# Kernel tuning notes

Measured on AMD Instinct MI355X. Metric: run time of the kernel, lower is better.

The kernel has to match this reference:

```python
import jax, jax.numpy as jnp
from jax import lax
import numpy as np

B, T, C = 32, 1024, 512
K = 3
MAX_DUR = 4            # durations drawn from [0,5) -> max value 4
L_MAX = T * MAX_DUR    # static padded mel length (torch pads to batch max; we pad to static max)
EPS = 1e-5


def conv_ln_block(x, w, b, g, beta):
    # x: [B,T,C]; torch ConvLNBlock: permute -> Conv1d(SAME) -> relu -> permute -> LayerNorm -> dropout(eval=id)
    y = lax.conv_general_dilated(x.transpose(0, 2, 1), w, (1,), 'SAME',
                                 dimension_numbers=('NCH', 'OIH', 'NCH')) + b[None, :, None]
    y = jax.nn.relu(y).transpose(0, 2, 1)  # [B,T,Cout]
    mu = y.mean(-1, keepdims=True)
    var = y.var(-1, keepdims=True)
    return (y - mu) * lax.rsqrt(var + EPS) * g + beta


def regulate(batch, durations, token_lengths):
    # Vectorized equivalent of DurationRegulator.inflate: repeat token t durations[b,t] times,
    # concatenate, pad. Implemented as cumsum + searchsorted gather (single pass, no ragged loops).
    pos = jnp.arange(T)
    valid = pos[None, :] < token_lengths[:, None]          # [B,T]
    d = jnp.where(valid, durations, 0)
    total = d.sum(axis=1)
    # torch: if durs.sum()==0 -> fill with 1
    d = jnp.where((total == 0)[:, None], valid.astype(d.dtype), d)
    total = d.sum(axis=1)                                   # [B]
    cum = jnp.cumsum(d, axis=1)                             # inclusive cumsum [B,T]
    frames = jnp.arange(L_MAX)
    idx = jax.vmap(lambda c: jnp.searchsorted(c, frames, side='right'))(cum)  # [B,L_MAX]
    idx = jnp.clip(idx, 0, T - 1)
    out = jnp.take_along_axis(batch, idx[:, :, None], axis=1)                 # [B,L_MAX,C]
    frame_mask = frames[None, :] < total[:, None]
    out = out * frame_mask[:, :, None].astype(batch.dtype)
    return out, total.astype(jnp.float32)


def setup_inputs() -> dict:
    key = jax.random.key(0)
    ks = jax.random.split(key, 8)
    batch = jax.random.normal(ks[0], (B, T, C), dtype=jnp.float32)
    token_lengths = jax.random.randint(ks[1], (B,), T // 2, T + 1).astype(jnp.int32)
    mask = jnp.arange(T)[None, :] < token_lengths[:, None]
    label_durations = jax.random.randint(ks[2], (B, T), 0, MAX_DUR + 1).astype(jnp.int32)
    s1 = 1.0 / np.sqrt(C * K)
    s2 = 1.0 / np.sqrt(C * K)
    params = {
        'conv1_w': jax.random.uniform(ks[3], (C, C, K), minval=-s1, maxval=s1, dtype=jnp.float32),
        'conv1_b': jnp.zeros((C,), jnp.float32),
        'ln1_g': jnp.ones((C,), jnp.float32), 'ln1_b': jnp.zeros((C,), jnp.float32),
        'conv2_w': jax.random.uniform(ks[4], (C, C, K), minval=-s2, maxval=s2, dtype=jnp.float32),
        'conv2_b': jnp.zeros((C,), jnp.float32),
        'ln2_g': jnp.ones((C,), jnp.float32), 'ln2_b': jnp.zeros((C,), jnp.float32),
        'lin_w': jax.random.uniform(ks[5], (C, 1), minval=-1/np.sqrt(C), maxval=1/np.sqrt(C), dtype=jnp.float32),
        'lin_b': jnp.zeros((1,), jnp.float32),
    }
    return dict(batch=batch, token_lengths=token_lengths, mask=mask,
                label_durations=label_durations, **params)


def reference(batch, token_lengths, mask, label_durations,
              conv1_w, conv1_b, ln1_g, ln1_b,
              conv2_w, conv2_b, ln2_g, ln2_b,
              lin_w, lin_b):
    # VariancePredictor: two ConvLN blocks + Linear(out_channels, 1), masked fill 0
    h = conv_ln_block(batch, conv1_w, conv1_b, ln1_g, ln1_b)
    h = conv_ln_block(h, conv2_w, conv2_b, ln2_g, ln2_b)
    predicted_durations = h @ lin_w + lin_b                      # [B,T,1]
    predicted_durations = jnp.where(mask[:, :, None], predicted_durations, 0.0)
    # label_durations provided -> regulator uses labels (training path), alpha=1
    padded_batch, mel_lengths = regulate(batch, label_durations, token_lengths)
    return padded_batch, mel_lengths, predicted_durations
```

## Files before the change

### kernel.cpp

```cpp
#include <hip/hip_runtime.h>
#include <hip/hip_bf16.h>
#include <stdint.h>

typedef _Float16 f16;
typedef _Float16 f16x8 __attribute__((ext_vector_type(8)));
typedef float f32x4 __attribute__((ext_vector_type(4)));

#define B_    32
#define T_    1024
#define TP_   1026
#define C_    512
#define LMAX_ 4096
#define KDIM  1536

#define XPAD_OFF   0u
#define H1PAD_OFF  33619968u
#define W1T_OFF    67239936u
#define W2T_OFF    68812800u
#define YWS_OFF    70385664u
#define CUM_OFF    137494528u
#define TOT_OFF    137625600u
#define IDX_OFF    137625728u

#define AS1C(p) ((const __attribute__((address_space(1))) void*)(p))
#define AS3(p)  ((__attribute__((address_space(3))) void*)(p))

__global__ __launch_bounds__(256) void prep_pad(const float* __restrict__ batch,
                                                f16* __restrict__ xpad,
                                                f16* __restrict__ h1pad) {
    int row = blockIdx.x * 4 + (threadIdx.x >> 6);
    int lane = threadIdx.x & 63;
    int b = row / TP_, tt = row % TP_;
    size_t dsto = (size_t)row * C_ + lane * 8;
    if (tt == 0 || tt == TP_ - 1) {
        f16x8 z = {};
        *(f16x8*)(xpad + dsto) = z;
        *(f16x8*)(h1pad + dsto) = z;
    } else {
        const float* src = batch + ((size_t)(b * T_ + tt - 1)) * C_ + lane * 8;
        float4 v0 = ((const float4*)src)[0];
        float4 v1 = ((const float4*)src)[1];
        f16x8 h;
        h[0] = (f16)v0.x; h[1] = (f16)v0.y; h[2] = (f16)v0.z; h[3] = (f16)v0.w;
        h[4] = (f16)v1.x; h[5] = (f16)v1.y; h[6] = (f16)v1.z; h[7] = (f16)v1.w;
        *(f16x8*)(xpad + dsto) = h;
    }
}

__global__ __launch_bounds__(256) void prep_w(const float* __restrict__ w1,
                                              const float* __restrict__ w2,
                                              f16* __restrict__ w1t,
                                              f16* __restrict__ w2t) {
    int o = blockIdx.x;
    const float* w = blockIdx.y ? w2 : w1;
    f16* wt = blockIdx.y ? w2t : w1t;
    for (int j = threadIdx.x; j < KDIM; j += 256) {
        int tap = j >> 9, i = j & 511;
        wt[(size_t)o * KDIM + j] = (f16)w[(size_t)o * KDIM + i * 3 + tap];
    }
}

__global__ __launch_bounds__(1024) void scan_kernel(const int* __restrict__ dur,
                                                    const int* __restrict__ tlen,
                                                    int* __restrict__ idxarr,
                                                    int* __restrict__ total,
                                                    float* __restrict__ mel_out) {
    int b = blockIdx.x, t = threadIdx.x;
    __shared__ int sd[1024];
    __shared__ int sv[1024];
    int L = tlen[b];
    int valid = (t < L) ? 1 : 0;
    int d = valid ? dur[b * T_ + t] : 0;
    sd[t] = d; sv[t] = valid;
    __syncthreads();
    for (int off = 1; off < 1024; off <<= 1) {
        int x = 0, y = 0;
        if (t >= off) { x = sd[t - off]; y = sv[t - off]; }
        __syncthreads();
        sd[t] += x; sv[t] += y;
        __syncthreads();
    }
    int totd = sd[1023];
    int cur  = (totd == 0) ? sv[t] : sd[t];
    int prev = (t == 0) ? 0 : ((totd == 0) ? sv[t - 1] : sd[t - 1]);
    for (int f = prev; f < cur; f++) idxarr[b * LMAX_ + f] = t;
    if (t == 1023) {
        int tt = (totd == 0) ? sv[1023] : totd;
        total[b] = tt;
        mel_out[b] = (float)tt;
    }
}

__global__ __launch_bounds__(256, 2) void gemm_convln(const f16* __restrict__ A,
                                                      const f16* __restrict__ Bw,
                                                      const float* __restrict__ bias,
                                                      float* __restrict__ Y) {
    __shared__ f16 As[128 * 64];
    __shared__ f16 Bs[128 * 64];
    const int tid = threadIdx.x;
    const int lane = tid & 63;
    const int wid = tid >> 6;
    const int m0 = blockIdx.x * 128;
    const int n0 = blockIdx.y * 128;
    const int arow0 = (m0 >> 10) * TP_ + (m0 & 1023);
    const int wm = (wid & 1) * 64;
    const int wn = (wid >> 1) * 64;

    f32x4 acc[4][4];
#pragma unroll
    for (int i = 0; i < 4; i++)
#pragma unroll
        for (int j = 0; j < 4; j++) acc[i][j] = (f32x4){0.f, 0.f, 0.f, 0.f};

    const int srow = wid * 8 + (lane >> 3);
    const int gmem = (lane & 7) ^ (lane >> 3);
    const f16* aBase = A + (size_t)(arow0 + srow) * C_ + gmem * 8;
    const f16* bBase = Bw + (size_t)(n0 + srow) * KDIM + gmem * 8;

    for (int kk = 0; kk < KDIM; kk += 64) {
        __syncthreads();
#pragma unroll
        for (int i = 0; i < 4; i++) {
            __builtin_amdgcn_global_load_lds(AS1C(aBase + (size_t)(i * 32) * C_ + kk),
                                             AS3(&As[(wid * 8 + i * 32) * 64]), 16, 0, 0);
            __builtin_amdgcn_global_load_lds(AS1C(bBase + (size_t)(i * 32) * KDIM + kk),
                                             AS3(&Bs[(wid * 8 + i * 32) * 64]), 16, 0, 0);
        }
        __syncthreads();
#pragma unroll
        for (int ks = 0; ks < 2; ks++) {
            const int slot = ((ks << 2) + (lane >> 4)) ^ (lane & 7);
            f16x8 af[4], bf[4];
#pragma unroll
            for (int mi = 0; mi < 4; mi++)
                af[mi] = *(const f16x8*)&As[(wm + mi * 16 + (lane & 15)) * 64 + slot * 8];
#pragma unroll
            for (int ni = 0; ni < 4; ni++)
                bf[ni] = *(const f16x8*)&Bs[(wn + ni * 16 + (lane & 15)) * 64 + slot * 8];
#pragma unroll
            for (int mi = 0; mi < 4; mi++)
#pragma unroll
                for (int ni = 0; ni < 4; ni++)
                    acc[mi][ni] = __builtin_amdgcn_mfma_f32_16x16x32_f16(
                        af[mi], bf[ni], acc[mi][ni], 0, 0, 0);
        }
    }

    const int col = lane & 15;
    const int row4 = (lane >> 4) * 4;
#pragma unroll
    for (int ni = 0; ni < 4; ni++) {
        int n = n0 + wn + ni * 16 + col;
        float bn = bias[n];
#pragma unroll
        for (int mi = 0; mi < 4; mi++) {
#pragma unroll
            for (int r = 0; r < 4; r++) {
                int m = m0 + wm + mi * 16 + row4 + r;
                float v = acc[mi][ni][r] + bn;
                Y[(size_t)m * C_ + n] = v > 0.f ? v : 0.f;
            }
        }
    }
}

__global__ __launch_bounds__(256) void ln_kernel(const float* __restrict__ Y,
                                                 const float* __restrict__ g,
                                                 const float* __restrict__ be,
                                                 f16* __restrict__ hpad) {
    int row = blockIdx.x * 4 + (threadIdx.x >> 6);
    int lane = threadIdx.x & 63;
    const float4* y = (const float4*)(Y + (size_t)row * C_);
    float4 v0 = y[lane * 2], v1 = y[lane * 2 + 1];
    float s = v0.x + v0.y + v0.z + v0.w + v1.x + v1.y + v1.z + v1.w;
    float q = v0.x * v0.x + v0.y * v0.y + v0.z * v0.z + v0.w * v0.w +
              v1.x * v1.x + v1.y * v1.y + v1.z * v1.z + v1.w * v1.w;
#pragma unroll
    for (int m = 32; m; m >>= 1) { s += __shfl_xor(s, m, 64); q += __shfl_xor(q, m, 64); }
    float mu = s * (1.f / 512.f);
    float x = q * (1.f / 512.f) - mu * mu + 1e-5f;
    float rs = rsqrtf(x);
    rs = rs * (1.5f - 0.5f * x * rs * rs);
    const float4* g4 = (const float4*)g;
    const float4* b4 = (const float4*)be;
    float4 g0 = g4[lane * 2], g1 = g4[lane * 2 + 1];
    float4 e0 = b4[lane * 2], e1 = b4[lane * 2 + 1];
    f16x8 h;
    h[0] = (f16)((v0.x - mu) * rs * g0.x + e0.x);
    h[1] = (f16)((v0.y - mu) * rs * g0.y + e0.y);
    h[2] = (f16)((v0.z - mu) * rs * g0.z + e0.z);
    h[3] = (f16)((v0.w - mu) * rs * g0.w + e0.w);
    h[4] = (f16)((v1.x - mu) * rs * g1.x + e1.x);
    h[5] = (f16)((v1.y - mu) * rs * g1.y + e1.y);
    h[6] = (f16)((v1.z - mu) * rs * g1.z + e1.z);
    h[7] = (f16)((v1.w - mu) * rs * g1.w + e1.w);
    int b = row >> 10, t = row & 1023;
    *(f16x8*)(hpad + ((size_t)(b * TP_ + t + 1)) * C_ + lane * 8) = h;
}

__global__ __launch_bounds__(256) void ln2pred_kernel(const float* __restrict__ Y,
                                                      const float* __restrict__ g,
                                                      const float* __restrict__ be,
                                                      const float* __restrict__ lw,
                                                      const float* __restrict__ lb,
                                                      const int* __restrict__ tlen,
                                                      float* __restrict__ pred) {
    int row = blockIdx.x * 4 + (threadIdx.x >> 6);
    int lane = threadIdx.x & 63;
    const float4* y = (const float4*)(Y + (size_t)row * C_);
    float4 v0 = y[lane * 2], v1 = y[lane * 2 + 1];
    float s = v0.x + v0.y + v0.z + v0.w + v1.x + v1.y + v1.z + v1.w;
    float q = v0.x * v0.x + v0.y * v0.y + v0.z * v0.z + v0.w * v0.w +
              v1.x * v1.x + v1.y * v1.y + v1.z * v1.z + v1.w * v1.w;
#pragma unroll
    for (int m = 32; m; m >>= 1) { s += __shfl_xor(s, m, 64); q += __shfl_xor(q, m, 64); }
    float mu = s * (1.f / 512.f);
    float x = q * (1.f / 512.f) - mu * mu + 1e-5f;
    float rs = rsqrtf(x);
    rs = rs * (1.5f - 0.5f * x * rs * rs);
    const float4* g4 = (const float4*)g;
    const float4* b4 = (const float4*)be;
    const float4* w4 = (const float4*)lw;
    float4 g0 = g4[lane * 2], g1 = g4[lane * 2 + 1];
    float4 e0 = b4[lane * 2], e1 = b4[lane * 2 + 1];
    float4 w0 = w4[lane * 2], w1 = w4[lane * 2 + 1];
    float p = ((v0.x - mu) * rs * g0.x + e0.x) * w0.x +
              ((v0.y - mu) * rs * g0.y + e0.y) * w0.y +
              ((v0.z - mu) * rs * g0.z + e0.z) * w0.z +
              ((v0.w - mu) * rs * g0.w + e0.w) * w0.w +
              ((v1.x - mu) * rs * g1.x + e1.x) * w1.x +
              ((v1.y - mu) * rs * g1.y + e1.y) * w1.y +
              ((v1.z - mu) * rs * g1.z + e1.z) * w1.z +
              ((v1.w - mu) * rs * g1.w + e1.w) * w1.w;
#pragma unroll
    for (int m = 32; m; m >>= 1) p += __shfl_xor(p, m, 64);
    if (lane == 0) {
        int b = row >> 10, t = row & 1023;
        pred[row] = (t < tlen[b]) ? (p + lb[0]) : 0.f;
    }
}

__global__ __launch_bounds__(256) void gather_kernel(const float* __restrict__ batch,
                                                     const int* __restrict__ idxarr,
                                                     const int* __restrict__ total,
                                                     float* __restrict__ out) {
    int gw = blockIdx.x * 4 + (threadIdx.x >> 6);
    int lane = threadIdx.x & 63;
    int b = gw >> 12;
    int l = gw & (LMAX_ - 1);
    int tot = total[b];
    float4* dst = (float4*)(out + ((size_t)b * LMAX_ + l) * C_);
    if (l < tot) {
        int idx = idxarr[gw];
        const float4* src = (const float4*)(batch + ((size_t)b * T_ + idx) * C_);
        dst[lane] = src[lane];
        dst[lane + 64] = src[lane + 64];
    } else {
        float4 z = {0.f, 0.f, 0.f, 0.f};
        dst[lane] = z;
        dst[lane + 64] = z;
    }
}

extern "C" void kernel_launch(void* const* d_in, const int* in_sizes, int n_in,
                              void* d_out, int out_size, void* d_ws, size_t ws_size,
                              hipStream_t stream) {
    const float* batch = (const float*)d_in[0];
    const int* tlen    = (const int*)d_in[1];
    const int* durs    = (const int*)d_in[3];
    const float* w1  = (const float*)d_in[4];
    const float* b1  = (const float*)d_in[5];
    const float* g1  = (const float*)d_in[6];
    const float* be1 = (const float*)d_in[7];
    const float* w2  = (const float*)d_in[8];
    const float* b2  = (const float*)d_in[9];
    const float* g2  = (const float*)d_in[10];
    const float* be2 = (const float*)d_in[11];
    const float* lw  = (const float*)d_in[12];
    const float* lb  = (const float*)d_in[13];

    float* out      = (float*)d_out;
    float* mel_out  = out + (size_t)B_ * LMAX_ * C_;
    float* pred_out = mel_out + B_;

    char* ws    = (char*)d_ws;
    f16* xpad   = (f16*)(ws + XPAD_OFF);
    f16* h1pad  = (f16*)(ws + H1PAD_OFF);
    f16* w1t    = (f16*)(ws + W1T_OFF);
    f16* w2t    = (f16*)(ws + W2T_OFF);
    float* yws  = (float*)(ws + YWS_OFF);
    int* tot    = (int*)(ws + TOT_OFF);
    int* idxarr = (int*)(ws + IDX_OFF);

    prep_pad<<<B_ * TP_ / 4, 256, 0, stream>>>(batch, xpad, h1pad);
    prep_w<<<dim3(512, 2), 256, 0, stream>>>(w1, w2, w1t, w2t);
    scan_kernel<<<B_, 1024, 0, stream>>>(durs, tlen, idxarr, tot, mel_out);
    gemm_convln<<<dim3(256, 4), 256, 0, stream>>>(xpad, w1t, b1, yws);
    ln_kernel<<<8192, 256, 0, stream>>>(yws, g1, be1, h1pad);
    gemm_convln<<<dim3(256, 4), 256, 0, stream>>>(h1pad, w2t, b2, yws);
    ln2pred_kernel<<<8192, 256, 0, stream>>>(yws, g2, be2, lw, lb, tlen, pred_out);
    gather_kernel<<<B_ * LMAX_ / 4, 256, 0, stream>>>(batch, idxarr, tot, out);
}
```

Baseline: 489.1 us.

## Fuse LayerNorm and prediction epilogues into full-row conv GEMM tiles

Each GEMM block now computes a 64-row by full 512-column tile using 32x32x16 MFMAs, so the LayerNorm (and, in the second pass, the linear prediction head) runs in the epilogue out of a shared-memory staging buffer. The fp32 intermediate workspace and the two separate LayerNorm kernels go away, which removes a large global write and read of the activations plus two launches. In exchange, each block uses about 72KB of LDS and a larger accumulator set, and the B tile per k-step is much larger. This may reduce occupancy, and the grid shrinks to 512 blocks.

```diff
diff --git a/kernel.cpp b/kernel.cpp
--- a/kernel.cpp
+++ b/kernel.cpp
@@ -3,8 +3,10 @@
 #include <stdint.h>
 
 typedef _Float16 f16;
+typedef _Float16 f16x4v __attribute__((ext_vector_type(4)));
 typedef _Float16 f16x8 __attribute__((ext_vector_type(8)));
 typedef float f32x4 __attribute__((ext_vector_type(4)));
+typedef float f32x16 __attribute__((ext_vector_type(16)));
 
 #define B_    32
 #define T_    1024
@@ -17,10 +19,8 @@
 #define H1PAD_OFF  33619968u
 #define W1T_OFF    67239936u
 #define W2T_OFF    68812800u
-#define YWS_OFF    70385664u
-#define CUM_OFF    137494528u
-#define TOT_OFF    137625600u
-#define IDX_OFF    137625728u
+#define TOT_OFF    70385664u
+#define IDX_OFF    70385920u
 
 #define AS1C(p) ((const __attribute__((address_space(1))) void*)(p))
 #define AS3(p)  ((__attribute__((address_space(3))) void*)(p))
@@ -91,152 +91,134 @@
     }
 }
 
-__global__ __launch_bounds__(256, 2) void gemm_convln(const f16* __restrict__ A,
-                                                      const f16* __restrict__ Bw,
-                                                      const float* __restrict__ bias,
-                                                      float* __restrict__ Y) {
-    __shared__ f16 As[128 * 64];
-    __shared__ f16 Bs[128 * 64];
+template <int MODE>
+__global__ __launch_bounds__(256, 2) void fgemm(const f16* __restrict__ A,
+                                                const f16* __restrict__ Bw,
+                                                const float* __restrict__ bias,
+                                                const float* __restrict__ g,
+                                                const float* __restrict__ be,
+                                                const float* __restrict__ lw,
+                                                const float* __restrict__ lb,
+                                                const int* __restrict__ tlen,
+                                                f16* __restrict__ hpad,
+                                                float* __restrict__ pred) {
+    __shared__ __align__(16) char smem[73728];
+    f16* As = (f16*)smem;
+    f16* Bs = (f16*)(smem + 8192);
+    float* Ew = (float*)smem;
+
     const int tid = threadIdx.x;
     const int lane = tid & 63;
-    const int wid = tid >> 6;
-    const int m0 = blockIdx.x * 128;
-    const int n0 = blockIdx.y * 128;
+    const int w = tid >> 6;
+    const int m0 = blockIdx.x * 64;
     const int arow0 = (m0 >> 10) * TP_ + (m0 & 1023);
-    const int wm = (wid & 1) * 64;
-    const int wn = (wid >> 1) * 64;
-
-    f32x4 acc[4][4];
-#pragma unroll
-    for (int i = 0; i < 4; i++)
-#pragma unroll
-        for (int j = 0; j < 4; j++) acc[i][j] = (f32x4){0.f, 0.f, 0.f, 0.f};
-
-    const int srow = wid * 8 + (lane >> 3);
-    const int gmem = (lane & 7) ^ (lane >> 3);
-    const f16* aBase = A + (size_t)(arow0 + srow) * C_ + gmem * 8;
-    const f16* bBase = Bw + (size_t)(n0 + srow) * KDIM + gmem * 8;
+
+    f32x16 acc[2][4];
+#pragma unroll
+    for (int i = 0; i < 2; i++)
+#pragma unroll
+        for (int j = 0; j < 4; j++) acc[i][j] = (f32x16){};
+
+    const int srow = lane >> 3;
+    const int gran = (lane & 7) ^ srow;
+    const f16* aB = A + (size_t)(arow0 + w * 16 + srow) * C_ + gran * 8;
+    const f16* bB = Bw + (size_t)(w * 128 + srow) * KDIM + gran * 8;
 
     for (int kk = 0; kk < KDIM; kk += 64) {
         __syncthreads();
 #pragma unroll
-        for (int i = 0; i < 4; i++) {
-            __builtin_amdgcn_global_load_lds(AS1C(aBase + (size_t)(i * 32) * C_ + kk),
-                                             AS3(&As[(wid * 8 + i * 32) * 64]), 16, 0, 0);
-            __builtin_amdgcn_global_load_lds(AS1C(bBase + (size_t)(i * 32) * KDIM + kk),
-                                             AS3(&Bs[(wid * 8 + i * 32) * 64]), 16, 0, 0);
+        for (int i = 0; i < 2; i++)
+            __builtin_amdgcn_global_load_lds(AS1C(aB + (size_t)(i * 8) * C_ + kk),
+                                             AS3(&As[(w * 16 + i * 8) * 64]), 16, 0, 0);
+#pragma unroll
+        for (int j = 0; j < 16; j++)
+            __builtin_amdgcn_global_load_lds(AS1C(bB + (size_t)(j * 8) * KDIM + kk),
+                                             AS3(&Bs[(w * 128 + j * 8) * 64]), 16, 0, 0);
+        __syncthreads();
+#pragma unroll
+        for (int ks = 0; ks < 4; ks++) {
+            const int slot = (ks * 2 + (lane >> 5)) ^ (lane & 7);
+            f16x8 af[2], bf[4];
+#pragma unroll
+            for (int mt = 0; mt < 2; mt++)
+                af[mt] = *(const f16x8*)&As[(mt * 32 + (lane & 31)) * 64 + slot * 8];
+#pragma unroll
+            for (int nt = 0; nt < 4; nt++)
+                bf[nt] = *(const f16x8*)&Bs[(w * 128 + nt * 32 + (lane & 31)) * 64 + slot * 8];
+#pragma unroll
+            for (int mt = 0; mt < 2; mt++)
+#pragma unroll
+                for (int nt = 0; nt < 4; nt++)
+                    acc[mt][nt] = __builtin_amdgcn_mfma_f32_32x32x16_f16(
+                        af[mt], bf[nt], acc[mt][nt], 0, 0, 0);
         }
-        __syncthreads();
-#pragma unroll
-        for (int ks = 0; ks < 2; ks++) {
-            const int slot = ((ks << 2) + (lane >> 4)) ^ (lane & 7);
-            f16x8 af[4], bf[4];
-#pragma unroll
-            for (int mi = 0; mi < 4; mi++)
-                af[mi] = *(const f16x8*)&As[(wm + mi * 16 + (lane & 15)) * 64 + slot * 8];
-#pragma unroll
-            for (int ni = 0; ni < 4; ni++)
-                bf[ni] = *(const f16x8*)&Bs[(wn + ni * 16 + (lane & 15)) * 64 + slot * 8];
-#pragma unroll
-            for (int mi = 0; mi < 4; mi++)
-#pragma unroll
-                for (int ni = 0; ni < 4; ni++)
-                    acc[mi][ni] = __builtin_amdgcn_mfma_f32_16x16x32_f16(
-                        af[mi], bf[ni], acc[mi][ni], 0, 0, 0);
-        }
-    }
-
-    const int col = lane & 15;
-    const int row4 = (lane >> 4) * 4;
-#pragma unroll
-    for (int ni = 0; ni < 4; ni++) {
-        int n = n0 + wn + ni * 16 + col;
-        float bn = bias[n];
-#pragma unroll
-        for (int mi = 0; mi < 4; mi++) {
-#pragma unroll
-            for (int r = 0; r < 4; r++) {
-                int m = m0 + wm + mi * 16 + row4 + r;
-                float v = acc[mi][ni][r] + bn;
-                Y[(size_t)m * C_ + n] = v > 0.f ? v : 0.f;
+    }
+
+    float bcol[4];
+#pragma unroll
+    for (int nt = 0; nt < 4; nt++) bcol[nt] = bias[w * 128 + nt * 32 + (lane & 31)];
+    const float4 gA = ((const float4*)g)[lane], gB = ((const float4*)g)[64 + lane];
+    const float4 eA = ((const float4*)be)[lane], eB = ((const float4*)be)[64 + lane];
+    float4 wA, wB;
+    if (MODE == 2) { wA = ((const float4*)lw)[lane]; wB = ((const float4*)lw)[64 + lane]; }
+
+#pragma unroll
+    for (int c = 0; c < 2; c++) {
+        __syncthreads();
+#pragma unroll
+        for (int nt = 0; nt < 4; nt++) {
+            const int col = w * 128 + nt * 32 + (lane & 31);
+#pragma unroll
+            for (int reg = 0; reg < 16; reg++) {
+                const int row = (reg & 3) + 8 * (reg >> 2) + 4 * (lane >> 5);
+                float v = acc[c][nt][reg] + bcol[nt];
+                Ew[row * 512 + col] = v > 0.f ? v : 0.f;
             }
         }
-    }
-}
-
-__global__ __launch_bounds__(256) void ln_kernel(const float* __restrict__ Y,
-                                                 const float* __restrict__ g,
-                                                 const float* __restrict__ be,
-                                                 f16* __restrict__ hpad) {
-    int row = blockIdx.x * 4 + (threadIdx.x >> 6);
-    int lane = threadIdx.x & 63;
-    const float4* y = (const float4*)(Y + (size_t)row * C_);
-    float4 v0 = y[lane * 2], v1 = y[lane * 2 + 1];
-    float s = v0.x + v0.y + v0.z + v0.w + v1.x + v1.y + v1.z + v1.w;
-    float q = v0.x * v0.x + v0.y * v0.y + v0.z * v0.z + v0.w * v0.w +
-              v1.x * v1.x + v1.y * v1.y + v1.z * v1.z + v1.w * v1.w;
-#pragma unroll
-    for (int m = 32; m; m >>= 1) { s += __shfl_xor(s, m, 64); q += __shfl_xor(q, m, 64); }
-    float mu = s * (1.f / 512.f);
-    float x = q * (1.f / 512.f) - mu * mu + 1e-5f;
-    float rs = rsqrtf(x);
-    rs = rs * (1.5f - 0.5f * x * rs * rs);
-    const float4* g4 = (const float4*)g;
-    const float4* b4 = (const float4*)be;
-    float4 g0 = g4[lane * 2], g1 = g4[lane * 2 + 1];
-    float4 e0 = b4[lane * 2], e1 = b4[lane * 2 + 1];
-    f16x8 h;
-    h[0] = (f16)((v0.x - mu) * rs * g0.x + e0.x);
-    h[1] = (f16)((v0.y - mu) * rs * g0.y + e0.y);
-    h[2] = (f16)((v0.z - mu) * rs * g0.z + e0.z);
-    h[3] = (f16)((v0.w - mu) * rs * g0.w + e0.w);
-    h[4] = (f16)((v1.x - mu) * rs * g1.x + e1.x);
-    h[5] = (f16)((v1.y - mu) * rs * g1.y + e1.y);
-    h[6] = (f16)((v1.z - mu) * rs * g1.z + e1.z);
-    h[7] = (f16)((v1.w - mu) * rs * g1.w + e1.w);
-    int b = row >> 10, t = row & 1023;
-    *(f16x8*)(hpad + ((size_t)(b * TP_ + t + 1)) * C_ + lane * 8) = h;
-}
-
-__global__ __launch_bounds__(256) void ln2pred_kernel(const float* __restrict__ Y,
-                                                      const float* __restrict__ g,
-                                                      const float* __restrict__ be,
-                                                      const float* __restrict__ lw,
-                                                      const float* __restrict__ lb,
-                                                      const int* __restrict__ tlen,
-                                                      float* __restrict__ pred) {
-    int row = blockIdx.x * 4 + (threadIdx.x >> 6);
-    int lane = threadIdx.x & 63;
-    const float4* y = (const float4*)(Y + (size_t)row * C_);
-    float4 v0 = y[lane * 2], v1 = y[lane * 2 + 1];
-    float s = v0.x + v0.y + v0.z + v0.w + v1.x + v1.y + v1.z + v1.w;
-    float q = v0.x * v0.x + v0.y * v0.y + v0.z * v0.z + v0.w * v0.w +
-              v1.x * v1.x + v1.y * v1.y + v1.z * v1.z + v1.w * v1.w;
-#pragma unroll
-    for (int m = 32; m; m >>= 1) { s += __shfl_xor(s, m, 64); q += __shfl_xor(q, m, 64); }
-    float mu = s * (1.f / 512.f);
-    float x = q * (1.f / 512.f) - mu * mu + 1e-5f;
-    float rs = rsqrtf(x);
-    rs = rs * (1.5f - 0.5f * x * rs * rs);
-    const float4* g4 = (const float4*)g;
-    const float4* b4 = (const float4*)be;
-    const float4* w4 = (const float4*)lw;
-    float4 g0 = g4[lane * 2], g1 = g4[lane * 2 + 1];
-    float4 e0 = b4[lane * 2], e1 = b4[lane * 2 + 1];
-    float4 w0 = w4[lane * 2], w1 = w4[lane * 2 + 1];
-    float p = ((v0.x - mu) * rs * g0.x + e0.x) * w0.x +
-              ((v0.y - mu) * rs * g0.y + e0.y) * w0.y +
-              ((v0.z - mu) * rs * g0.z + e0.z) * w0.z +
-              ((v0.w - mu) * rs * g0.w + e0.w) * w0.w +
-              ((v1.x - mu) * rs * g1.x + e1.x) * w1.x +
-              ((v1.y - mu) * rs * g1.y + e1.y) * w1.y +
-              ((v1.z - mu) * rs * g1.z + e1.z) * w1.z +
-              ((v1.w - mu) * rs * g1.w + e1.w) * w1.w;
-#pragma unroll
-    for (int m = 32; m; m >>= 1) p += __shfl_xor(p, m, 64);
-    if (lane == 0) {
-        int b = row >> 10, t = row & 1023;
-        pred[row] = (t < tlen[b]) ? (p + lb[0]) : 0.f;
+        __syncthreads();
+#pragma unroll
+        for (int i = 0; i < 8; i++) {
+            const int r = w + i * 4;
+            float4 v0 = *(const float4*)&Ew[r * 512 + lane * 4];
+            float4 v1 = *(const float4*)&Ew[r * 512 + 256 + lane * 4];
+            float s = v0.x + v0.y + v0.z + v0.w + v1.x + v1.y + v1.z + v1.w;
+            float q = v0.x * v0.x + v0.y * v0.y + v0.z * v0.z + v0.w * v0.w +
+                      v1.x * v1.x + v1.y * v1.y + v1.z * v1.z + v1.w * v1.w;
+#pragma unroll
+            for (int m = 32; m; m >>= 1) { s += __shfl_xor(s, m, 64); q += __shfl_xor(q, m, 64); }
+            float mu = s * (1.f / 512.f);
+            float x = q * (1.f / 512.f) - mu * mu + 1e-5f;
+            float rs = rsqrtf(x);
+            rs = rs * (1.5f - 0.5f * x * rs * rs);
+            const int m = m0 + c * 32 + r;
+            const int b = m >> 10, t = m & 1023;
+            if (MODE == 1) {
+                f16x4v h0, h1;
+                h0[0] = (f16)((v0.x - mu) * rs * gA.x + eA.x);
+                h0[1] = (f16)((v0.y - mu) * rs * gA.y + eA.y);
+                h0[2] = (f16)((v0.z - mu) * rs * gA.z + eA.z);
+                h0[3] = (f16)((v0.w - mu) * rs * gA.w + eA.w);
+                h1[0] = (f16)((v1.x - mu) * rs * gB.x + eB.x);
+                h1[1] = (f16)((v1.y - mu) * rs * gB.y + eB.y);
+                h1[2] = (f16)((v1.z - mu) * rs * gB.z + eB.z);
+                h1[3] = (f16)((v1.w - mu) * rs * gB.w + eB.w);
+                f16* dst = hpad + ((size_t)(b * TP_ + t + 1)) * C_;
+                *(f16x4v*)(dst + lane * 4) = h0;
+                *(f16x4v*)(dst + 256 + lane * 4) = h1;
+            } else {
+                float p = ((v0.x - mu) * rs * gA.x + eA.x) * wA.x +
+                          ((v0.y - mu) * rs * gA.y + eA.y) * wA.y +
+                          ((v0.z - mu) * rs * gA.z + eA.z) * wA.z +
+                          ((v0.w - mu) * rs * gA.w + eA.w) * wA.w +
+                          ((v1.x - mu) * rs * gB.x + eB.x) * wB.x +
+                          ((v1.y - mu) * rs * gB.y + eB.y) * wB.y +
+                          ((v1.z - mu) * rs * gB.z + eB.z) * wB.z +
+                          ((v1.w - mu) * rs * gB.w + eB.w) * wB.w;
+#pragma unroll
+                for (int mm = 32; mm; mm >>= 1) p += __shfl_xor(p, mm, 64);
+                if (lane == 0) pred[m] = (t < tlen[b]) ? (p + lb[0]) : 0.f;
+            }
+        }
     }
 }
 
@@ -288,16 +270,15 @@
     f16* h1pad  = (f16*)(ws + H1PAD_OFF);
     f16* w1t    = (f16*)(ws + W1T_OFF);
     f16* w2t    = (f16*)(ws + W2T_OFF);
-    float* yws  = (float*)(ws + YWS_OFF);
     int* tot    = (int*)(ws + TOT_OFF);
     int* idxarr = (int*)(ws + IDX_OFF);
 
     prep_pad<<<B_ * TP_ / 4, 256, 0, stream>>>(batch, xpad, h1pad);
     prep_w<<<dim3(512, 2), 256, 0, stream>>>(w1, w2, w1t, w2t);
     scan_kernel<<<B_, 1024, 0, stream>>>(durs, tlen, idxarr, tot, mel_out);
-    gemm_convln<<<dim3(256, 4), 256, 0, stream>>>(xpad, w1t, b1, yws);
-    ln_kernel<<<8192, 256, 0, stream>>>(yws, g1, be1, h1pad);
-    gemm_convln<<<dim3(256, 4), 256, 0, stream>>>(h1pad, w2t, b2, yws);
-    ln2pred_kernel<<<8192, 256, 0, stream>>>(yws, g2, be2, lw, lb, tlen, pred_out);
+    fgemm<1><<<512, 256, 0, stream>>>(xpad, w1t, b1, g1, be1, nullptr, nullptr, nullptr,
+                                      h1pad, nullptr);
+    fgemm<2><<<512, 256, 0, stream>>>(h1pad, w2t, b2, g2, be2, lw, lb, tlen,
+                                      nullptr, pred_out);
     gather_kernel<<<B_ * LMAX_ / 4, 256, 0, stream>>>(batch, idxarr, tot, out);
 }
```

New measurement: 490.2 us. About the same (+0.2%).
